# Optimization experiments

Measured on AMD Instinct MI355X. Metric: run time of the kernel, lower is better.

Reference implementation:

```python
import jax, jax.numpy as jnp
import numpy as np

N_QUBITS = 10
N_LATENT = 6
N_LAYERS = 2
AMP_DIM = 2 ** N_QUBITS  # 1024


def _apply_1q(state, gate, q):
    # state: [B] + [2]*N_QUBITS complex; gate: [2,2]; wire q -> axis q+1 (wire 0 = MSB)
    s = jnp.tensordot(gate, state, axes=[[1], [q + 1]])  # new axis at front
    return jnp.moveaxis(s, 0, q + 1)


def _ry_mat(theta):
    c = jnp.cos(theta / 2)
    s = jnp.sin(theta / 2)
    return jnp.stack([jnp.stack([c, -s]), jnp.stack([s, c])]).astype(jnp.complex64)


def _rz_mat(theta):
    half = theta / 2
    e = jnp.cos(half) + 1j * jnp.sin(half)  # e^{i theta/2}
    zero = jnp.zeros((), jnp.complex64)
    return jnp.stack([jnp.stack([jnp.conj(e), zero]), jnp.stack([zero, e])]).astype(jnp.complex64)


def _cnot(state, c, t):
    # flip target axis where control bit == 1
    ctrl_shape = [1] * (N_QUBITS + 1)
    ctrl_shape[c + 1] = 2
    ctrl = jnp.arange(2).reshape(ctrl_shape)
    return jnp.where(ctrl == 1, jnp.flip(state, axis=t + 1), state)


def _expvals(state):
    # PauliX, PauliY, PauliZ on wires 0..N_LATENT-1  -> [B, 3*N_LATENT]
    rest = tuple(range(1, N_QUBITS))  # axes of the 9 remaining wires after a take
    xs, ys, zs = [], [], []
    for q in range(N_LATENT):
        s0 = jnp.take(state, 0, axis=q + 1)
        s1 = jnp.take(state, 1, axis=q + 1)
        z01 = jnp.conj(s0) * s1
        xs.append(2.0 * jnp.sum(z01.real, axis=rest))
        ys.append(2.0 * jnp.sum(z01.imag, axis=rest))
        zs.append(jnp.sum(jnp.abs(s0) ** 2 - jnp.abs(s1) ** 2, axis=rest))
    return jnp.stack(xs + ys + zs, axis=1)


def _simulate(x, weights):
    B, D = x.shape
    if D < AMP_DIM:
        x = jnp.pad(x, ((0, 0), (0, AMP_DIM - D)))
    else:
        x = x[:, :AMP_DIM]
    norm = jnp.maximum(jnp.linalg.norm(x, axis=-1, keepdims=True), 1e-8)
    x = x / norm
    state = x.astype(jnp.complex64).reshape((B,) + (2,) * N_QUBITS)
    for layer in range(N_LAYERS):
        off = layer * N_QUBITS * 3
        for q in range(N_QUBITS):
            state = _apply_1q(state, _ry_mat(weights[off + q]), q)
        for q in range(N_QUBITS):
            state = _apply_1q(state, _rz_mat(weights[off + N_QUBITS + q]), q)
        for q in range(N_QUBITS):
            state = _cnot(state, q, (q + 1) % N_QUBITS)
        for q in range(N_QUBITS):
            state = _apply_1q(state, _ry_mat(weights[off + 2 * N_QUBITS + q]), q)
    return _expvals(state).astype(jnp.float32)


def setup_inputs() -> dict:
    key = jax.random.key(0)
    k1, k2 = jax.random.split(key)
    B, D = 32768, 768
    x = jax.random.normal(k1, (B, D), dtype=jnp.float32)
    std = np.sqrt(2.0 / (N_QUBITS + N_LAYERS)).astype(np.float32)
    weights = jax.random.normal(k2, (N_LAYERS * N_QUBITS * 3,), dtype=jnp.float32) * std
    return {"x": x, "weights": weights}


def reference(x, weights):
    return _simulate(x, weights)
```

## Files before the change

### kernel.cpp

```cpp
#include <hip/hip_runtime.h>

#define DIN 768

typedef float f2 __attribute__((ext_vector_type(2)));
typedef int i2v __attribute__((ext_vector_type(2)));

#if __has_builtin(__builtin_amdgcn_permlane32_swap)
#define HAVE_PL32 1
#endif
#if __has_builtin(__builtin_amdgcn_permlane16_swap)
#define HAVE_PL16 1
#endif

__device__ __forceinline__ int f2i(float v) { return __builtin_bit_cast(int, v); }
__device__ __forceinline__ float i2f(int v) { return __builtin_bit_cast(float, v); }

template<int CTRL>
__device__ __forceinline__ float dppf(float v) {
  const int i = f2i(v);
  return i2f(__builtin_amdgcn_update_dpp(i, i, CTRL, 0xF, 0xF, true));
}
template<int CTRL>
__device__ __forceinline__ f2 dppf2(f2 v) {
  f2 r; r.x = dppf<CTRL>(v.x); r.y = dppf<CTRL>(v.y); return r;
}

__device__ __forceinline__ f2 wsum2(f2 v) {
  v += dppf2<0xB1>(v);
  v += dppf2<0x4E>(v);
  v += dppf2<0x124>(v);
  v += dppf2<0x128>(v);
#ifdef HAVE_PL16
  { i2v rx = __builtin_amdgcn_permlane16_swap(f2i(v.x), f2i(v.x), false, false);
    i2v ry = __builtin_amdgcn_permlane16_swap(f2i(v.y), f2i(v.y), false, false);
    v.x = i2f(rx.x) + i2f(rx.y);
    v.y = i2f(ry.x) + i2f(ry.y); }
#else
  v.x += __shfl_xor(v.x, 16); v.y += __shfl_xor(v.y, 16);
#endif
#ifdef HAVE_PL32
  { i2v rx = __builtin_amdgcn_permlane32_swap(f2i(v.x), f2i(v.x), false, false);
    i2v ry = __builtin_amdgcn_permlane32_swap(f2i(v.y), f2i(v.y), false, false);
    v.x = i2f(rx.x) + i2f(rx.y);
    v.y = i2f(ry.x) + i2f(ry.y); }
#else
  v.x += __shfl_xor(v.x, 32); v.y += __shfl_xor(v.y, 32);
#endif
  return v;
}

template<int MASK>
__device__ __forceinline__ f2 shflx_f2(f2 v, int lane) {
  f2 r;
  if constexpr (MASK == 1) {
    r = dppf2<0xB1>(v);
  } else if constexpr (MASK == 2) {
    r = dppf2<0x4E>(v);
  } else if constexpr (MASK == 16) {
#ifdef HAVE_PL16
    const i2v a = __builtin_amdgcn_permlane16_swap(f2i(v.x), f2i(v.x), false, false);
    const i2v b = __builtin_amdgcn_permlane16_swap(f2i(v.y), f2i(v.y), false, false);
    const bool hi = (lane >> 4) & 1;
    r.x = hi ? i2f(a.x) : i2f(a.y);
    r.y = hi ? i2f(b.x) : i2f(b.y);
#else
    r.x = __shfl_xor(v.x, 16); r.y = __shfl_xor(v.y, 16);
#endif
  } else if constexpr (MASK == 32) {
#ifdef HAVE_PL32
    const i2v a = __builtin_amdgcn_permlane32_swap(f2i(v.x), f2i(v.x), false, false);
    const i2v b = __builtin_amdgcn_permlane32_swap(f2i(v.y), f2i(v.y), false, false);
    const bool lo = lane < 32;
    r.x = lo ? i2f(a.y) : i2f(a.x);
    r.y = lo ? i2f(b.y) : i2f(b.x);
#else
    r.x = __shfl_xor(v.x, 32); r.y = __shfl_xor(v.y, 32);
#endif
  } else {
    r.x = __shfl_xor(v.x, MASK); r.y = __shfl_xor(v.y, MASK);
  }
  return r;
}

__device__ __forceinline__ int swz(int i) { return i ^ ((i >> 4) & 31); }

__device__ __forceinline__ int cnotL(int i) {
  const int b9 = (i >> 9) & 1;
  const int b8 = (i >> 8) & 1;
  const int b0 = i & 1;
  return ((i ^ (i >> 1)) & 0xFF) | ((b8 ^ b9 ^ b0) << 8) | ((b9 ^ b0) << 9);
}

template<int RB>
__device__ __forceinline__ void ry1(f2 (&a)[16], float c, float s) {
#pragma unroll
  for (int r = 0; r < 16; ++r) {
    if (!(r & (1 << RB))) {
      const int p = r | (1 << RB);
      const f2 a0 = a[r], a1 = a[p];
      a[r] = a0 * c - a1 * s;
      a[p] = a1 * c + a0 * s;
    }
  }
}
template<int RB>
__device__ __forceinline__ void ry2(f2 (&re)[16], f2 (&im)[16], float c, float s) {
  ry1<RB>(re, c, s);
  ry1<RB>(im, c, s);
}
template<int MASK>
__device__ __forceinline__ void ry1_shfl(int lane, f2 (&a)[16], float c, float s) {
  const float ss = (lane & MASK) ? s : -s;
#pragma unroll
  for (int r = 0; r < 16; ++r) {
    const f2 p = shflx_f2<MASK>(a[r], lane);
    a[r] = a[r] * c + p * ss;
  }
}

template<int RB>
__device__ __forceinline__ void xyr(const f2 (&re)[16], const f2 (&im)[16], f2& aX, f2& aY) {
#pragma unroll
  for (int r = 0; r < 16; ++r) {
    if (!(r & (1 << RB))) {
      const int p = r | (1 << RB);
      aX += re[r] * re[p] + im[r] * im[p];
      aY += re[r] * im[p] - im[r] * re[p];
    }
  }
}
template<int MASK>
__device__ __forceinline__ void xys(int lane, const f2 (&re)[16], const f2 (&im)[16], f2& aX, f2& aY) {
  const float sgn = (lane & MASK) ? -1.f : 1.f;
#pragma unroll
  for (int r = 0; r < 16; ++r) {
    const f2 pr = shflx_f2<MASK>(re[r], lane);
    const f2 pi = shflx_f2<MASK>(im[r], lane);
    aX += re[r] * pr + im[r] * pi;
    aY += (re[r] * pi - im[r] * pr) * sgn;
  }
}

__global__ void qae_prep(const float* __restrict__ w, float2* __restrict__ ws) {
  const int i = threadIdx.x;
  if (i < 50) {
    float s, c; __sincosf(0.5f * w[i], &s, &c);
    ws[i] = make_float2(c, s);
  } else if (i < 56) {
    float s, c; __sincosf(w[i], &s, &c);
    ws[i] = make_float2(c, s);
  } else if (i < 60) {
    ws[i] = make_float2(1.f, 0.f);
  } else if (i < 70) {
    const int q = i - 60;
    float s, c; __sincosf(0.5f * (w[20 + q] + w[30 + q]), &s, &c);
    ws[i] = make_float2(c, s);
  }
  float p1 = 0.f, p2 = 0.f;
#pragma unroll
  for (int b = 0; b < 10; ++b) {
    const float sg = ((i >> b) & 1) ? 0.5f : -0.5f;
    p1 += sg * w[10 + 9 - b];
    p2 += sg * w[40 + 9 - b];
  }
  float s, c;
  __sincosf(p1, &s, &c); ws[70 + i]        = make_float2(c, s);
  __sincosf(p2, &s, &c); ws[70 + 1024 + i] = make_float2(c, s);
}

__global__ __launch_bounds__(128) void qae_main(const float* __restrict__ x,
                                                const float2* __restrict__ gt,
                                                float* __restrict__ out, int Btot) {
  __shared__ f2 lds[2 * 1024];
  const int tid  = threadIdx.x;
  const int lane = tid & 63;
  const int wid  = tid >> 6;
  const int gw   = blockIdx.x * 2 + wid;
  const int b0   = gw * 2, b1 = b0 + 1;
  if (b0 >= Btot) return;
  const bool has1 = (b1 < Btot);
  f2* stc = lds + (wid << 10);
  const float2* rz1 = gt + 70;
  const float2* rz2 = gt + 70 + 1024;

  f2 g[16];
  f2 ss = (f2){0.f, 0.f};
  const float* x0 = x + (size_t)b0 * DIN;
  const float* x1 = x + (size_t)b1 * DIN;
#pragma unroll
  for (int t = 0; t < 4; ++t) {
    const int idx = lane * 16 + 4 * t;
    float4 va = make_float4(0.f, 0.f, 0.f, 0.f);
    float4 vb = make_float4(0.f, 0.f, 0.f, 0.f);
    if (idx < DIN) {
      va = *reinterpret_cast<const float4*>(x0 + idx);
      if (has1) vb = *reinterpret_cast<const float4*>(x1 + idx);
    }
    g[4*t+0] = (f2){va.x, vb.x}; g[4*t+1] = (f2){va.y, vb.y};
    g[4*t+2] = (f2){va.z, vb.z}; g[4*t+3] = (f2){va.w, vb.w};
#pragma unroll
    for (int k = 0; k < 4; ++k) ss += g[4*t+k] * g[4*t+k];
  }
  ss = wsum2(ss);
  const f2 inv = (f2){1.f / fmaxf(ss.x, 1e-16f), 1.f / fmaxf(ss.y, 1e-16f)};

  float2 cs;
  cs = gt[6]; ry1<3>(g, cs.x, cs.y);
  cs = gt[7]; ry1<2>(g, cs.x, cs.y);
  cs = gt[8]; ry1<1>(g, cs.x, cs.y);
  cs = gt[9]; ry1<0>(g, cs.x, cs.y);
  cs = gt[4]; ry1_shfl<2>(lane, g, cs.x, cs.y);
  cs = gt[5]; ry1_shfl<1>(lane, g, cs.x, cs.y);

#pragma unroll
  for (int r = 0; r < 16; ++r) stc[swz((lane << 4) | r)] = g[r];
#pragma unroll
  for (int r = 0; r < 16; ++r) g[r] = stc[swz((r << 6) | lane)];

  cs = gt[0]; ry1<3>(g, cs.x, cs.y);
  cs = gt[1]; ry1<2>(g, cs.x, cs.y);
  cs = gt[2]; ry1<1>(g, cs.x, cs.y);
  cs = gt[3]; ry1<0>(g, cs.x, cs.y);

  f2 re[16], im[16];
#pragma unroll
  for (int r = 0; r < 16; ++r) {
    const float2 t = rz1[(r << 6) | lane];
    re[r] = g[r] * t.x;
    im[r] = g[r] * t.y;
  }

#pragma unroll
  for (int r = 0; r < 16; ++r) stc[swz((r << 6) | lane)] = re[r];
#pragma unroll
  for (int r = 0; r < 16; ++r) re[r] = stc[swz(cnotL((lane << 4) | r))];
#pragma unroll
  for (int r = 0; r < 16; ++r) stc[swz((r << 6) | lane)] = im[r];
#pragma unroll
  for (int r = 0; r < 16; ++r) im[r] = stc[swz(cnotL((lane << 4) | r))];

  cs = gt[66]; ry2<3>(re, im, cs.x, cs.y);
  cs = gt[67]; ry2<2>(re, im, cs.x, cs.y);
  cs = gt[68]; ry2<1>(re, im, cs.x, cs.y);
  cs = gt[69]; ry2<0>(re, im, cs.x, cs.y);
  cs = gt[64]; ry1_shfl<2>(lane, re, cs.x, cs.y); ry1_shfl<2>(lane, im, cs.x, cs.y);
  cs = gt[65]; ry1_shfl<1>(lane, re, cs.x, cs.y); ry1_shfl<1>(lane, im, cs.x, cs.y);

#pragma unroll
  for (int r = 0; r < 16; ++r) stc[swz((lane << 4) | r)] = re[r];
#pragma unroll
  for (int r = 0; r < 16; ++r) re[r] = stc[swz((r << 6) | lane)];
#pragma unroll
  for (int r = 0; r < 16; ++r) stc[swz((lane << 4) | r)] = im[r];
#pragma unroll
  for (int r = 0; r < 16; ++r) im[r] = stc[swz((r << 6) | lane)];

  cs = gt[60]; ry2<3>(re, im, cs.x, cs.y);
  cs = gt[61]; ry2<2>(re, im, cs.x, cs.y);
  cs = gt[62]; ry2<1>(re, im, cs.x, cs.y);
  cs = gt[63]; ry2<0>(re, im, cs.x, cs.y);

#pragma unroll
  for (int r = 0; r < 16; ++r) {
    const float2 t = rz2[(r << 6) | lane];
    const f2 nre = re[r] * t.x - im[r] * t.y;
    im[r] = re[r] * t.y + im[r] * t.x;
    re[r] = nre;
  }

#pragma unroll
  for (int r = 0; r < 16; ++r) stc[swz((r << 6) | lane)] = re[r];
#pragma unroll
  for (int r = 0; r < 16; ++r) re[r] = stc[swz(cnotL((r << 6) | lane))];
#pragma unroll
  for (int r = 0; r < 16; ++r) stc[swz((r << 6) | lane)] = im[r];
#pragma unroll
  for (int r = 0; r < 16; ++r) im[r] = stc[swz(cnotL((r << 6) | lane))];

  f2 a18[18];
#pragma unroll
  for (int k = 0; k < 12; ++k) a18[k] = (f2){0.f, 0.f};

  {
    f2 psum = (f2){0.f, 0.f};
    f2 z0 = (f2){0.f,0.f}, z1 = (f2){0.f,0.f}, z2 = (f2){0.f,0.f}, z3 = (f2){0.f,0.f};
#pragma unroll
    for (int r = 0; r < 16; ++r) {
      const f2 p = re[r] * re[r] + im[r] * im[r];
      psum += p;
      z0 += (r & 8) ? -p : p;
      z1 += (r & 4) ? -p : p;
      z2 += (r & 2) ? -p : p;
      z3 += (r & 1) ? -p : p;
    }
    a18[12] = z0; a18[13] = z1; a18[14] = z2; a18[15] = z3;
    a18[16] = ((lane >> 5) & 1) ? -psum : psum;
    a18[17] = ((lane >> 4) & 1) ? -psum : psum;
  }

  xyr<3>(re, im, a18[0], a18[6]);
  xyr<2>(re, im, a18[1], a18[7]);
  xyr<1>(re, im, a18[2], a18[8]);
  xyr<0>(re, im, a18[3], a18[9]);
  xys<32>(lane, re, im, a18[4], a18[10]);
  xys<16>(lane, re, im, a18[5], a18[11]);

#pragma unroll
  for (int k = 0; k < 18; ++k) {
    f2 v = a18[k];
    v += dppf2<0xB1>(v);
    v += dppf2<0x4E>(v);
    a18[k] = v;
  }
  float* red = reinterpret_cast<float*>(stc);
  if ((lane & 3) == 0) {
    const int q = lane >> 2;
    f2* redf2 = reinterpret_cast<f2*>(red);
#pragma unroll
    for (int k = 0; k < 18; ++k) redf2[q * 18 + k] = a18[k];
  }
  if (lane < 36) {
    const int c  = (lane >= 18) ? 1 : 0;
    const int j  = lane - 18 * c;
    const int jq = (j < 6) ? j : ((j < 12) ? j - 6 : j - 12);
    const int jp = (j < 6) ? (j + 12) : ((j >= 12) ? (j - 12) : j);
    float S = 0.f, P = 0.f;
#pragma unroll
    for (int q = 0; q < 16; ++q) {
      S += red[(q * 18 + j ) * 2 + c];
      P += red[(q * 18 + jp) * 2 + c];
    }
    const float fac  = (jq < 4) ? 2.f : 1.f;
    const float2 fa  = gt[50 + jq];
    const float invc = c ? inv.y : inv.x;
    float o;
    if (j < 6)       o = (fac * S * fa.x + P * fa.y) * invc;
    else if (j < 12) o = fac * S * invc;
    else             o = (S * fa.x - fac * P * fa.y) * invc;
    if (c == 0 || has1) out[(size_t)(b0 + c) * 18 + j] = o;
  }
}

extern "C" void kernel_launch(void* const* d_in, const int* in_sizes, int n_in,
                              void* d_out, int out_size, void* d_ws, size_t ws_size,
                              hipStream_t stream) {
  const float* x = (const float*)d_in[0];
  const float* w = (const float*)d_in[1];
  float* out = (float*)d_out;
  float2* ws = (float2*)d_ws;
  const int B = in_sizes[0] / DIN;
  qae_prep<<<dim3(1), dim3(1024), 0, stream>>>(w, ws);
  const int grid = (B + 3) / 4;
  qae_main<<<dim3(grid), dim3(128), 0, stream>>>(x, (const float2*)ws, out, B);
}
```

Measured before the change: 106.4 us.

## Split each sample pair across two waves with 8 amplitudes per lane

Each 1024-amplitude state pair is now spread across a 128-thread block, two wavefronts with 8 amplitudes per lane, where before a single wave held 16 per lane. Qubit-to-lane mapping changes so lane-local gates use DPP and ds_swizzle in place of permlane swaps, and LDS transposes now need block-level barriers. The intent is lower register pressure and higher occupancy (launch bounds 128,8), at the cost of extra __syncthreads and cross-wave reductions through LDS.

```diff
diff --git a/kernel.cpp b/kernel.cpp
--- a/kernel.cpp
+++ b/kernel.cpp
@@ -49,40 +49,14 @@
   return v;
 }
 
-template<int MASK>
-__device__ __forceinline__ f2 shflx_f2(f2 v, int lane) {
+__device__ __forceinline__ f2 swz4_f2(f2 v) {
   f2 r;
-  if constexpr (MASK == 1) {
-    r = dppf2<0xB1>(v);
-  } else if constexpr (MASK == 2) {
-    r = dppf2<0x4E>(v);
-  } else if constexpr (MASK == 16) {
-#ifdef HAVE_PL16
-    const i2v a = __builtin_amdgcn_permlane16_swap(f2i(v.x), f2i(v.x), false, false);
-    const i2v b = __builtin_amdgcn_permlane16_swap(f2i(v.y), f2i(v.y), false, false);
-    const bool hi = (lane >> 4) & 1;
-    r.x = hi ? i2f(a.x) : i2f(a.y);
-    r.y = hi ? i2f(b.x) : i2f(b.y);
-#else
-    r.x = __shfl_xor(v.x, 16); r.y = __shfl_xor(v.y, 16);
-#endif
-  } else if constexpr (MASK == 32) {
-#ifdef HAVE_PL32
-    const i2v a = __builtin_amdgcn_permlane32_swap(f2i(v.x), f2i(v.x), false, false);
-    const i2v b = __builtin_amdgcn_permlane32_swap(f2i(v.y), f2i(v.y), false, false);
-    const bool lo = lane < 32;
-    r.x = lo ? i2f(a.y) : i2f(a.x);
-    r.y = lo ? i2f(b.y) : i2f(b.x);
-#else
-    r.x = __shfl_xor(v.x, 32); r.y = __shfl_xor(v.y, 32);
-#endif
-  } else {
-    r.x = __shfl_xor(v.x, MASK); r.y = __shfl_xor(v.y, MASK);
-  }
+  r.x = i2f(__builtin_amdgcn_ds_swizzle(f2i(v.x), 0x101F));
+  r.y = i2f(__builtin_amdgcn_ds_swizzle(f2i(v.y), 0x101F));
   return r;
 }
 
-__device__ __forceinline__ int swz(int i) { return i ^ ((i >> 4) & 31); }
+__device__ __forceinline__ int swz(int j) { return j ^ ((j >> 4) & 15); }
 
 __device__ __forceinline__ int cnotL(int i) {
   const int b9 = (i >> 9) & 1;
@@ -91,10 +65,16 @@
   return ((i ^ (i >> 1)) & 0xFF) | ((b8 ^ b9 ^ b0) << 8) | ((b9 ^ b0) << 9);
 }
 
+__device__ __forceinline__ int bmap(int sl) {
+  const int l = sl & 63, h = sl >> 6;
+  return (((l >> 1) & 1) << 6) | ((l & 1) << 5) | (((l >> 2) & 1) << 4) |
+         (((l >> 3) & 1) << 3) | (((l >> 4) & 1) << 2) | (((l >> 5) & 1) << 1) | h;
+}
+
 template<int RB>
-__device__ __forceinline__ void ry1(f2 (&a)[16], float c, float s) {
-#pragma unroll
-  for (int r = 0; r < 16; ++r) {
+__device__ __forceinline__ void ry8(f2 (&a)[8], float c, float s) {
+#pragma unroll
+  for (int r = 0; r < 8; ++r) {
     if (!(r & (1 << RB))) {
       const int p = r | (1 << RB);
       const f2 a0 = a[r], a1 = a[p];
@@ -103,59 +83,32 @@
     }
   }
 }
-template<int RB>
-__device__ __forceinline__ void ry2(f2 (&re)[16], f2 (&im)[16], float c, float s) {
-  ry1<RB>(re, c, s);
-  ry1<RB>(im, c, s);
-}
-template<int MASK>
-__device__ __forceinline__ void ry1_shfl(int lane, f2 (&a)[16], float c, float s) {
-  const float ss = (lane & MASK) ? s : -s;
-#pragma unroll
-  for (int r = 0; r < 16; ++r) {
-    const f2 p = shflx_f2<MASK>(a[r], lane);
-    a[r] = a[r] * c + p * ss;
-  }
-}
-
-template<int RB>
-__device__ __forceinline__ void xyr(const f2 (&re)[16], const f2 (&im)[16], f2& aX, f2& aY) {
-#pragma unroll
-  for (int r = 0; r < 16; ++r) {
-    if (!(r & (1 << RB))) {
-      const int p = r | (1 << RB);
-      aX += re[r] * re[p] + im[r] * im[p];
-      aY += re[r] * im[p] - im[r] * re[p];
-    }
-  }
-}
-template<int MASK>
-__device__ __forceinline__ void xys(int lane, const f2 (&re)[16], const f2 (&im)[16], f2& aX, f2& aY) {
-  const float sgn = (lane & MASK) ? -1.f : 1.f;
-#pragma unroll
-  for (int r = 0; r < 16; ++r) {
-    const f2 pr = shflx_f2<MASK>(re[r], lane);
-    const f2 pi = shflx_f2<MASK>(im[r], lane);
-    aX += re[r] * pr + im[r] * pi;
-    aY += (re[r] * pi - im[r] * pr) * sgn;
+template<int CTRL>
+__device__ __forceinline__ void ry8_dpp(f2 (&a)[8], float c, float ssgn) {
+#pragma unroll
+  for (int r = 0; r < 8; ++r) {
+    const f2 p = dppf2<CTRL>(a[r]);
+    a[r] = a[r] * c + p * ssgn;
   }
 }
 
 __global__ void qae_prep(const float* __restrict__ w, float2* __restrict__ ws) {
-  const int i = threadIdx.x;
-  if (i < 50) {
-    float s, c; __sincosf(0.5f * w[i], &s, &c);
-    ws[i] = make_float2(c, s);
-  } else if (i < 56) {
-    float s, c; __sincosf(w[i], &s, &c);
-    ws[i] = make_float2(c, s);
-  } else if (i < 60) {
-    ws[i] = make_float2(1.f, 0.f);
-  } else if (i < 70) {
-    const int q = i - 60;
+  const int k = threadIdx.x;
+  if (k < 50) {
+    float s, c; __sincosf(0.5f * w[k], &s, &c);
+    ws[k] = make_float2(c, s);
+  } else if (k < 56) {
+    float s, c; __sincosf(w[k], &s, &c);
+    ws[k] = make_float2(c, s);
+  } else if (k < 60) {
+    ws[k] = make_float2(1.f, 0.f);
+  } else if (k < 70) {
+    const int q = k - 60;
     float s, c; __sincosf(0.5f * (w[20 + q] + w[30 + q]), &s, &c);
-    ws[i] = make_float2(c, s);
-  }
+    ws[60 + q] = make_float2(c, s);
+  }
+  const int r  = k >> 7, sl = k & 127;
+  const int i  = (r << 7) | bmap(sl);
   float p1 = 0.f, p2 = 0.f;
 #pragma unroll
   for (int b = 0; b < 10; ++b) {
@@ -164,179 +117,247 @@
     p2 += sg * w[40 + 9 - b];
   }
   float s, c;
-  __sincosf(p1, &s, &c); ws[70 + i]        = make_float2(c, s);
-  __sincosf(p2, &s, &c); ws[70 + 1024 + i] = make_float2(c, s);
-}
-
-__global__ __launch_bounds__(128) void qae_main(const float* __restrict__ x,
-                                                const float2* __restrict__ gt,
-                                                float* __restrict__ out, int Btot) {
-  __shared__ f2 lds[2 * 1024];
-  const int tid  = threadIdx.x;
-  const int lane = tid & 63;
-  const int wid  = tid >> 6;
-  const int gw   = blockIdx.x * 2 + wid;
-  const int b0   = gw * 2, b1 = b0 + 1;
-  if (b0 >= Btot) return;
-  const bool has1 = (b1 < Btot);
-  f2* stc = lds + (wid << 10);
+  __sincosf(p1, &s, &c); ws[70 + k]        = make_float2(c, s);
+  __sincosf(p2, &s, &c); ws[70 + 1024 + k] = make_float2(c, s);
+}
+
+__global__ __launch_bounds__(128, 8) void qae_main(const float* __restrict__ x,
+                                                   const float2* __restrict__ gt,
+                                                   float* __restrict__ out, int Btot) {
+  __shared__ f2 st[1026];
+  const int sl   = threadIdx.x;
+  const int lane = sl & 63;
+  const int h    = sl >> 6;
+  const int b0   = blockIdx.x * 2;
+  const bool has1 = (b0 + 1 < Btot);
+  const int bm   = bmap(sl);
+  const int base = sl << 3;
   const float2* rz1 = gt + 70;
   const float2* rz2 = gt + 70 + 1024;
 
-  f2 g[16];
+  f2 re[8], im[8];
   f2 ss = (f2){0.f, 0.f};
   const float* x0 = x + (size_t)b0 * DIN;
-  const float* x1 = x + (size_t)b1 * DIN;
-#pragma unroll
-  for (int t = 0; t < 4; ++t) {
-    const int idx = lane * 16 + 4 * t;
+  const float* x1 = x + (size_t)(b0 + 1) * DIN;
+#pragma unroll
+  for (int t = 0; t < 2; ++t) {
+    const int idx = base + 4 * t;
     float4 va = make_float4(0.f, 0.f, 0.f, 0.f);
     float4 vb = make_float4(0.f, 0.f, 0.f, 0.f);
     if (idx < DIN) {
       va = *reinterpret_cast<const float4*>(x0 + idx);
       if (has1) vb = *reinterpret_cast<const float4*>(x1 + idx);
     }
-    g[4*t+0] = (f2){va.x, vb.x}; g[4*t+1] = (f2){va.y, vb.y};
-    g[4*t+2] = (f2){va.z, vb.z}; g[4*t+3] = (f2){va.w, vb.w};
-#pragma unroll
-    for (int k = 0; k < 4; ++k) ss += g[4*t+k] * g[4*t+k];
+    re[4*t+0] = (f2){va.x, vb.x}; re[4*t+1] = (f2){va.y, vb.y};
+    re[4*t+2] = (f2){va.z, vb.z}; re[4*t+3] = (f2){va.w, vb.w};
+#pragma unroll
+    for (int k = 0; k < 4; ++k) ss += re[4*t+k] * re[4*t+k];
   }
   ss = wsum2(ss);
-  const f2 inv = (f2){1.f / fmaxf(ss.x, 1e-16f), 1.f / fmaxf(ss.y, 1e-16f)};
+  if (lane == 0) st[1024 + h] = ss;
 
   float2 cs;
-  cs = gt[6]; ry1<3>(g, cs.x, cs.y);
-  cs = gt[7]; ry1<2>(g, cs.x, cs.y);
-  cs = gt[8]; ry1<1>(g, cs.x, cs.y);
-  cs = gt[9]; ry1<0>(g, cs.x, cs.y);
-  cs = gt[4]; ry1_shfl<2>(lane, g, cs.x, cs.y);
-  cs = gt[5]; ry1_shfl<1>(lane, g, cs.x, cs.y);
-
-#pragma unroll
-  for (int r = 0; r < 16; ++r) stc[swz((lane << 4) | r)] = g[r];
-#pragma unroll
-  for (int r = 0; r < 16; ++r) g[r] = stc[swz((r << 6) | lane)];
-
-  cs = gt[0]; ry1<3>(g, cs.x, cs.y);
-  cs = gt[1]; ry1<2>(g, cs.x, cs.y);
-  cs = gt[2]; ry1<1>(g, cs.x, cs.y);
-  cs = gt[3]; ry1<0>(g, cs.x, cs.y);
-
-  f2 re[16], im[16];
-#pragma unroll
-  for (int r = 0; r < 16; ++r) {
-    const float2 t = rz1[(r << 6) | lane];
-    re[r] = g[r] * t.x;
-    im[r] = g[r] * t.y;
-  }
-
-#pragma unroll
-  for (int r = 0; r < 16; ++r) stc[swz((r << 6) | lane)] = re[r];
-#pragma unroll
-  for (int r = 0; r < 16; ++r) re[r] = stc[swz(cnotL((lane << 4) | r))];
-#pragma unroll
-  for (int r = 0; r < 16; ++r) stc[swz((r << 6) | lane)] = im[r];
-#pragma unroll
-  for (int r = 0; r < 16; ++r) im[r] = stc[swz(cnotL((lane << 4) | r))];
-
-  cs = gt[66]; ry2<3>(re, im, cs.x, cs.y);
-  cs = gt[67]; ry2<2>(re, im, cs.x, cs.y);
-  cs = gt[68]; ry2<1>(re, im, cs.x, cs.y);
-  cs = gt[69]; ry2<0>(re, im, cs.x, cs.y);
-  cs = gt[64]; ry1_shfl<2>(lane, re, cs.x, cs.y); ry1_shfl<2>(lane, im, cs.x, cs.y);
-  cs = gt[65]; ry1_shfl<1>(lane, re, cs.x, cs.y); ry1_shfl<1>(lane, im, cs.x, cs.y);
-
-#pragma unroll
-  for (int r = 0; r < 16; ++r) stc[swz((lane << 4) | r)] = re[r];
-#pragma unroll
-  for (int r = 0; r < 16; ++r) re[r] = stc[swz((r << 6) | lane)];
-#pragma unroll
-  for (int r = 0; r < 16; ++r) stc[swz((lane << 4) | r)] = im[r];
-#pragma unroll
-  for (int r = 0; r < 16; ++r) im[r] = stc[swz((r << 6) | lane)];
-
-  cs = gt[60]; ry2<3>(re, im, cs.x, cs.y);
-  cs = gt[61]; ry2<2>(re, im, cs.x, cs.y);
-  cs = gt[62]; ry2<1>(re, im, cs.x, cs.y);
-  cs = gt[63]; ry2<0>(re, im, cs.x, cs.y);
-
-#pragma unroll
-  for (int r = 0; r < 16; ++r) {
-    const float2 t = rz2[(r << 6) | lane];
+  cs = gt[7]; ry8<2>(re, cs.x, cs.y);
+  cs = gt[8]; ry8<1>(re, cs.x, cs.y);
+  cs = gt[9]; ry8<0>(re, cs.x, cs.y);
+  cs = gt[5]; ry8_dpp<0x4E>(re, cs.x, (lane & 2) ? cs.y : -cs.y);
+  cs = gt[6]; ry8_dpp<0xB1>(re, cs.x, (lane & 1) ? cs.y : -cs.y);
+
+#pragma unroll
+  for (int r = 0; r < 8; ++r) st[swz(base + r)] = re[r];
+  __syncthreads();
+#pragma unroll
+  for (int r = 0; r < 8; ++r) re[r] = st[swz((r << 7) | bm)];
+  __syncthreads();
+
+  cs = gt[0]; ry8<2>(re, cs.x, cs.y);
+  cs = gt[1]; ry8<1>(re, cs.x, cs.y);
+  cs = gt[2]; ry8<0>(re, cs.x, cs.y);
+  cs = gt[3]; ry8_dpp<0x4E>(re, cs.x, (lane & 2) ? cs.y : -cs.y);
+  cs = gt[4]; ry8_dpp<0xB1>(re, cs.x, (lane & 1) ? cs.y : -cs.y);
+
+#pragma unroll
+  for (int r = 0; r < 8; ++r) {
+    const float2 t = rz1[(r << 7) | sl];
+    im[r] = re[r] * t.y;
+    re[r] = re[r] * t.x;
+  }
+
+#pragma unroll
+  for (int r = 0; r < 8; ++r) st[swz((r << 7) | bm)] = re[r];
+  __syncthreads();
+#pragma unroll
+  for (int r = 0; r < 8; ++r) re[r] = st[swz(cnotL(base + r))];
+  __syncthreads();
+#pragma unroll
+  for (int r = 0; r < 8; ++r) st[swz((r << 7) | bm)] = im[r];
+  __syncthreads();
+#pragma unroll
+  for (int r = 0; r < 8; ++r) im[r] = st[swz(cnotL(base + r))];
+  __syncthreads();
+
+  cs = gt[67]; ry8<2>(re, cs.x, cs.y); ry8<2>(im, cs.x, cs.y);
+  cs = gt[68]; ry8<1>(re, cs.x, cs.y); ry8<1>(im, cs.x, cs.y);
+  cs = gt[69]; ry8<0>(re, cs.x, cs.y); ry8<0>(im, cs.x, cs.y);
+  { cs = gt[65]; const float sg = (lane & 2) ? cs.y : -cs.y;
+    ry8_dpp<0x4E>(re, cs.x, sg); ry8_dpp<0x4E>(im, cs.x, sg); }
+  { cs = gt[66]; const float sg = (lane & 1) ? cs.y : -cs.y;
+    ry8_dpp<0xB1>(re, cs.x, sg); ry8_dpp<0xB1>(im, cs.x, sg); }
+
+#pragma unroll
+  for (int r = 0; r < 8; ++r) st[swz(base + r)] = re[r];
+  __syncthreads();
+#pragma unroll
+  for (int r = 0; r < 8; ++r) re[r] = st[swz((r << 7) | bm)];
+  __syncthreads();
+#pragma unroll
+  for (int r = 0; r < 8; ++r) st[swz(base + r)] = im[r];
+  __syncthreads();
+#pragma unroll
+  for (int r = 0; r < 8; ++r) im[r] = st[swz((r << 7) | bm)];
+  __syncthreads();
+
+  cs = gt[60]; ry8<2>(re, cs.x, cs.y); ry8<2>(im, cs.x, cs.y);
+  cs = gt[61]; ry8<1>(re, cs.x, cs.y); ry8<1>(im, cs.x, cs.y);
+  cs = gt[62]; ry8<0>(re, cs.x, cs.y); ry8<0>(im, cs.x, cs.y);
+  { cs = gt[63]; const float sg = (lane & 2) ? cs.y : -cs.y;
+    ry8_dpp<0x4E>(re, cs.x, sg); ry8_dpp<0x4E>(im, cs.x, sg); }
+  { cs = gt[64]; const float sg = (lane & 1) ? cs.y : -cs.y;
+    ry8_dpp<0xB1>(re, cs.x, sg); ry8_dpp<0xB1>(im, cs.x, sg); }
+
+#pragma unroll
+  for (int r = 0; r < 8; ++r) {
+    const float2 t = rz2[(r << 7) | sl];
     const f2 nre = re[r] * t.x - im[r] * t.y;
     im[r] = re[r] * t.y + im[r] * t.x;
     re[r] = nre;
   }
 
 #pragma unroll
-  for (int r = 0; r < 16; ++r) stc[swz((r << 6) | lane)] = re[r];
-#pragma unroll
-  for (int r = 0; r < 16; ++r) re[r] = stc[swz(cnotL((r << 6) | lane))];
-#pragma unroll
-  for (int r = 0; r < 16; ++r) stc[swz((r << 6) | lane)] = im[r];
-#pragma unroll
-  for (int r = 0; r < 16; ++r) im[r] = stc[swz(cnotL((r << 6) | lane))];
-
-  f2 a18[18];
-#pragma unroll
-  for (int k = 0; k < 12; ++k) a18[k] = (f2){0.f, 0.f};
-
-  {
-    f2 psum = (f2){0.f, 0.f};
-    f2 z0 = (f2){0.f,0.f}, z1 = (f2){0.f,0.f}, z2 = (f2){0.f,0.f}, z3 = (f2){0.f,0.f};
-#pragma unroll
-    for (int r = 0; r < 16; ++r) {
+  for (int r = 0; r < 8; ++r) st[swz((r << 7) | bm)] = re[r];
+  __syncthreads();
+#pragma unroll
+  for (int r = 0; r < 8; ++r) re[r] = st[swz(cnotL((r << 7) | bm))];
+  __syncthreads();
+#pragma unroll
+  for (int r = 0; r < 8; ++r) st[swz((r << 7) | bm)] = im[r];
+  __syncthreads();
+#pragma unroll
+  for (int r = 0; r < 8; ++r) im[r] = st[swz(cnotL((r << 7) | bm))];
+  __syncthreads();
+
+  const int q16 = (h << 4) | (lane >> 2);
+  auto flush = [&](int j, f2 v) {
+    v += dppf2<0xB1>(v);
+    v += dppf2<0x4E>(v);
+    if (!(lane & 3)) st[q16 * 20 + j] = v;
+  };
+  const float s3 = (lane & 2) ? -1.f : 1.f;
+  const float s4 = (lane & 1) ? -1.f : 1.f;
+  const float s5 = (lane & 4) ? -1.f : 1.f;
+
+  {
+    f2 psum = (f2){0.f,0.f}, z0 = psum, z1 = psum, z2 = psum;
+#pragma unroll
+    for (int r = 0; r < 8; ++r) {
       const f2 p = re[r] * re[r] + im[r] * im[r];
       psum += p;
-      z0 += (r & 8) ? -p : p;
-      z1 += (r & 4) ? -p : p;
-      z2 += (r & 2) ? -p : p;
-      z3 += (r & 1) ? -p : p;
-    }
-    a18[12] = z0; a18[13] = z1; a18[14] = z2; a18[15] = z3;
-    a18[16] = ((lane >> 5) & 1) ? -psum : psum;
-    a18[17] = ((lane >> 4) & 1) ? -psum : psum;
-  }
-
-  xyr<3>(re, im, a18[0], a18[6]);
-  xyr<2>(re, im, a18[1], a18[7]);
-  xyr<1>(re, im, a18[2], a18[8]);
-  xyr<0>(re, im, a18[3], a18[9]);
-  xys<32>(lane, re, im, a18[4], a18[10]);
-  xys<16>(lane, re, im, a18[5], a18[11]);
-
-#pragma unroll
-  for (int k = 0; k < 18; ++k) {
-    f2 v = a18[k];
-    v += dppf2<0xB1>(v);
-    v += dppf2<0x4E>(v);
-    a18[k] = v;
-  }
-  float* red = reinterpret_cast<float*>(stc);
-  if ((lane & 3) == 0) {
-    const int q = lane >> 2;
-    f2* redf2 = reinterpret_cast<f2*>(red);
-#pragma unroll
-    for (int k = 0; k < 18; ++k) redf2[q * 18 + k] = a18[k];
-  }
-  if (lane < 36) {
-    const int c  = (lane >= 18) ? 1 : 0;
-    const int j  = lane - 18 * c;
+      z0 += (r & 4) ? -p : p;
+      z1 += (r & 2) ? -p : p;
+      z2 += (r & 1) ? -p : p;
+    }
+    flush(12, z0); flush(13, z1); flush(14, z2);
+    flush(15, psum * s3); flush(16, psum * s4); flush(17, psum * s5);
+  }
+  {
+    f2 aX = (f2){0.f,0.f}, aY = aX;
+#pragma unroll
+    for (int r = 0; r < 4; ++r) {
+      const int p = r + 4;
+      aX += re[r] * re[p] + im[r] * im[p];
+      aY += re[r] * im[p] - im[r] * re[p];
+    }
+    flush(0, aX); flush(6, aY);
+  }
+  {
+    f2 aX = (f2){0.f,0.f}, aY = aX;
+#pragma unroll
+    for (int r = 0; r < 8; ++r) if (!(r & 2)) {
+      const int p = r | 2;
+      aX += re[r] * re[p] + im[r] * im[p];
+      aY += re[r] * im[p] - im[r] * re[p];
+    }
+    flush(1, aX); flush(7, aY);
+  }
+  {
+    f2 aX = (f2){0.f,0.f}, aY = aX;
+#pragma unroll
+    for (int r = 0; r < 8; ++r) if (!(r & 1)) {
+      const int p = r | 1;
+      aX += re[r] * re[p] + im[r] * im[p];
+      aY += re[r] * im[p] - im[r] * re[p];
+    }
+    flush(2, aX); flush(8, aY);
+  }
+  {
+    f2 aX = (f2){0.f,0.f}, aY = aX;
+    const f2 sy = (f2){s3, s3};
+#pragma unroll
+    for (int r = 0; r < 8; ++r) {
+      const f2 pre = dppf2<0x4E>(re[r]);
+      const f2 pim = dppf2<0x4E>(im[r]);
+      aX += re[r] * pre + im[r] * pim;
+      aY += (re[r] * pim - im[r] * pre) * sy;
+    }
+    flush(3, aX); flush(9, aY);
+  }
+  {
+    f2 aX = (f2){0.f,0.f}, aY = aX;
+    const f2 sy = (f2){s4, s4};
+#pragma unroll
+    for (int r = 0; r < 8; ++r) {
+      const f2 pre = dppf2<0xB1>(re[r]);
+      const f2 pim = dppf2<0xB1>(im[r]);
+      aX += re[r] * pre + im[r] * pim;
+      aY += (re[r] * pim - im[r] * pre) * sy;
+    }
+    flush(4, aX); flush(10, aY);
+  }
+  {
+    f2 aX = (f2){0.f,0.f}, aY = aX;
+    const f2 sy = (f2){s5, s5};
+#pragma unroll
+    for (int r = 0; r < 8; ++r) {
+      const f2 pre = swz4_f2(re[r]);
+      const f2 pim = swz4_f2(im[r]);
+      aX += re[r] * pre + im[r] * pim;
+      aY += (re[r] * pim - im[r] * pre) * sy;
+    }
+    flush(5, aX); flush(11, aY);
+  }
+  __syncthreads();
+
+  if (sl < 36) {
+    const int c  = (sl >= 18) ? 1 : 0;
+    const int j  = sl - 18 * c;
     const int jq = (j < 6) ? j : ((j < 12) ? j - 6 : j - 12);
     const int jp = (j < 6) ? (j + 12) : ((j >= 12) ? (j - 12) : j);
+    const float* red = reinterpret_cast<const float*>(st);
     float S = 0.f, P = 0.f;
 #pragma unroll
-    for (int q = 0; q < 16; ++q) {
-      S += red[(q * 18 + j ) * 2 + c];
-      P += red[(q * 18 + jp) * 2 + c];
-    }
-    const float fac  = (jq < 4) ? 2.f : 1.f;
-    const float2 fa  = gt[50 + jq];
-    const float invc = c ? inv.y : inv.x;
+    for (int q = 0; q < 32; ++q) {
+      S += red[q * 40 + 2 * j  + c];
+      P += red[q * 40 + 2 * jp + c];
+    }
+    const float fac = (jq < 3) ? 2.f : 1.f;
+    const float2 fa = gt[50 + jq];
+    const f2 t0 = st[1024], t1 = st[1025];
+    const float tot = c ? (t0.y + t1.y) : (t0.x + t1.x);
+    const float inv = 1.f / fmaxf(tot, 1e-16f);
     float o;
-    if (j < 6)       o = (fac * S * fa.x + P * fa.y) * invc;
-    else if (j < 12) o = fac * S * invc;
-    else             o = (S * fa.x - fac * P * fa.y) * invc;
+    if (j < 6)       o = (fac * S * fa.x + P * fa.y) * inv;
+    else if (j < 12) o = fac * S * inv;
+    else             o = (S * fa.x - fac * P * fa.y) * inv;
     if (c == 0 || has1) out[(size_t)(b0 + c) * 18 + j] = o;
   }
 }
@@ -350,6 +371,6 @@
   float2* ws = (float2*)d_ws;
   const int B = in_sizes[0] / DIN;
   qae_prep<<<dim3(1), dim3(1024), 0, stream>>>(w, ws);
-  const int grid = (B + 3) / 4;
+  const int grid = (B + 1) / 2;
   qae_main<<<dim3(grid), dim3(128), 0, stream>>>(x, (const float2*)ws, out, B);
 }
```

Measured after the change: 135.7 us. 27.6% more time.
